# Kernel optimization log

Hardware: AMD Instinct MI355X
Metric: run time of the kernel (lower is better)

## Reference

```python
import jax, jax.numpy as jnp
import numpy as np

OUT_H, OUT_W = 7, 7
SPATIAL_SCALE = 0.25
SAMPLING_RATIO = 2  # fixed sampling grid per bin (sampling_ratio > 0 branch)


def setup_inputs() -> dict:
    key = jax.random.key(0)
    k1, k2, k3, k4, k5 = jax.random.split(key, 5)
    B, C, H, W = 2, 256, 200, 200
    N = 1000
    features = jax.random.normal(k1, (B, C, H, W), dtype=jnp.float32)
    # rois: [batch_idx, cx, cy, w, h, theta] in IMAGE coords (image = 800x800 since scale=0.25)
    batch_idx = jax.random.randint(k2, (N,), 0, B).astype(jnp.float32)
    centers = jax.random.uniform(k3, (N, 2), minval=100.0, maxval=700.0)
    sizes = jax.random.uniform(k4, (N, 2), minval=32.0, maxval=256.0)
    angles = jax.random.uniform(k5, (N, 1), minval=0.0, maxval=float(np.pi))
    rois = jnp.concatenate([batch_idx[:, None], centers, sizes, angles], axis=1).astype(jnp.float32)
    return {"features": features, "rois": rois}


def _roi_align_rotated(features, rois, out_h, out_w, scale, g):
    B, C, H, W = features.shape
    N = rois.shape[0]
    b = rois[:, 0].astype(jnp.int32)
    cx = rois[:, 1] * scale
    cy = rois[:, 2] * scale
    rw = jnp.maximum(rois[:, 3] * scale, 1.0)
    rh = jnp.maximum(rois[:, 4] * scale, 1.0)
    theta = rois[:, 5]
    bin_h = rh / out_h
    bin_w = rw / out_w
    # sample offsets within the roi: yy = -h/2 + (s + 0.5) * bin/g for s in [0, out*g)
    sy = (jnp.arange(out_h * g, dtype=features.dtype) + 0.5) / g  # [Hs] in bin units
    sx = (jnp.arange(out_w * g, dtype=features.dtype) + 0.5) / g  # [Ws]
    yy = -rh[:, None] * 0.5 + sy[None, :] * bin_h[:, None]  # [N, Hs]
    xx = -rw[:, None] * 0.5 + sx[None, :] * bin_w[:, None]  # [N, Ws]
    cos_t = jnp.cos(theta)[:, None, None]
    sin_t = jnp.sin(theta)[:, None, None]
    # rotate around roi center (mmcv / detectron2 convention)
    y = yy[:, :, None] * cos_t - xx[:, None, :] * sin_t + cy[:, None, None]  # [N, Hs, Ws]
    x = yy[:, :, None] * sin_t + xx[:, None, :] * cos_t + cx[:, None, None]
    # bilinear_interpolate semantics from the CUDA kernel
    inside = (y >= -1.0) & (y <= H) & (x >= -1.0) & (x <= W)
    yc = jnp.clip(y, 0.0)
    xc = jnp.clip(x, 0.0)
    yl = jnp.minimum(jnp.floor(yc).astype(jnp.int32), H - 1)
    xl = jnp.minimum(jnp.floor(xc).astype(jnp.int32), W - 1)
    yh = jnp.minimum(yl + 1, H - 1)
    xh = jnp.minimum(xl + 1, W - 1)
    ly = jnp.where(jnp.floor(yc) >= H - 1, 0.0, yc - yl)
    lx = jnp.where(jnp.floor(xc) >= W - 1, 0.0, xc - xl)
    hy = 1.0 - ly
    hx = 1.0 - lx
    bi = b[:, None, None]
    v1 = features[bi, :, yl, xl]  # [N, Hs, Ws, C]
    v2 = features[bi, :, yl, xh]
    v3 = features[bi, :, yh, xl]
    v4 = features[bi, :, yh, xh]
    w1 = (hy * hx)[..., None]
    w2 = (hy * lx)[..., None]
    w3 = (ly * hx)[..., None]
    w4 = (ly * lx)[..., None]
    val = w1 * v1 + w2 * v2 + w3 * v3 + w4 * v4
    val = jnp.where(inside[..., None], val, 0.0)
    # average over the g x g samples per output bin
    val = val.reshape(N, out_h, g, out_w, g, C).mean(axis=(2, 4))  # [N, out_h, out_w, C]
    return jnp.transpose(val, (0, 3, 1, 2))  # [N, C, out_h, out_w]


def reference(features, rois):
    return _roi_align_rotated(features, rois, OUT_H, OUT_W, SPATIAL_SCALE, SAMPLING_RATIO)
```

## Files before the change

kernel.cpp:

```cpp
#include <hip/hip_runtime.h>
#include <hip/hip_fp16.h>


#define B_ 2
#define C_ 256
#define H_ 200
#define W_ 200
#define OUTHW 7
#define GRID_S 14
#define NSAMP 196
#define ELEMS (C_ * OUTHW * OUTHW)

__global__ __launch_bounds__(256) void transpose_h_kernel(
    const float* __restrict__ feat, __half* __restrict__ featT)
{
    __shared__ float tile[64][65];
    const int x0   = blockIdx.x * 64;
    const int c0   = blockIdx.y * 64;
    const int yb   = blockIdx.z;
    const int y    = yb % H_;
    const int b    = yb / H_;
    const int t    = threadIdx.x;
    const int lane = t & 63;
    const int grp  = t >> 6;
    const int nx   = min(64, W_ - x0);

    if (lane < nx) {
        #pragma unroll
        for (int i = 0; i < 16; ++i) {
            const int cl = grp * 16 + i;
            tile[cl][lane] =
                feat[((size_t)(b * C_ + c0 + cl) * H_ + y) * W_ + x0 + lane];
        }
    }
    __syncthreads();

    for (int i = grp; i < nx; i += 4) {
        const float v = tile[lane][i];
        featT[((size_t)(b * H_ + y) * W_ + x0 + i) * C_ + c0 + lane] =
            __float2half(v);
    }
}

__device__ __forceinline__ void build_table(
    const float* __restrict__ rois, int n, int t,
    float s_w[4][NSAMP], int s_idx[4][NSAMP], int pix_stride, int fold_batch,
    int* s_b)
{
    const float spatial_scale = 0.25f;
    if (t == 0 && s_b) *s_b = (int)rois[n * 6 + 0];
    if (t < NSAMP) {
        const int   b  = (int)rois[n * 6 + 0];
        const float cx = rois[n * 6 + 1] * spatial_scale;
        const float cy = rois[n * 6 + 2] * spatial_scale;
        const float rw = fmaxf(rois[n * 6 + 3] * spatial_scale, 1.0f);
        const float rh = fmaxf(rois[n * 6 + 4] * spatial_scale, 1.0f);
        const float th = rois[n * 6 + 5];
        const float cosv = cosf(th), sinv = sinf(th);

        const float bin_h = rh * (1.0f / OUTHW);
        const float bin_w = rw * (1.0f / OUTHW);
        const int row = t / GRID_S;
        const int col = t % GRID_S;

        const float yy = -rh * 0.5f + ((float)row + 0.5f) * 0.5f * bin_h;
        const float xx = -rw * 0.5f + ((float)col + 0.5f) * 0.5f * bin_w;

        const float y = yy * cosv - xx * sinv + cy;
        const float x = yy * sinv + xx * cosv + cx;

        const bool inside = (y >= -1.0f) && (y <= (float)H_) &&
                            (x >= -1.0f) && (x <= (float)W_);

        const float yc = fmaxf(y, 0.0f);
        const float xc = fmaxf(x, 0.0f);
        const float fy = floorf(yc);
        const float fx = floorf(xc);
        int yl = min((int)fy, H_ - 1);
        int xl = min((int)fx, W_ - 1);
        const int yh = min(yl + 1, H_ - 1);
        const int xh = min(xl + 1, W_ - 1);
        const float ly = (fy >= (float)(H_ - 1)) ? 0.0f : (yc - fy);
        const float lx = (fx >= (float)(W_ - 1)) ? 0.0f : (xc - fx);
        const float hy = 1.0f - ly;
        const float hx = 1.0f - lx;

        const float m = inside ? 0.25f : 0.0f;
        s_w[0][t] = hy * hx * m;
        s_w[1][t] = hy * lx * m;
        s_w[2][t] = ly * hx * m;
        s_w[3][t] = ly * lx * m;
        const int bb = fold_batch ? b : 0;
        s_idx[0][t] = ((bb * H_ + yl) * W_ + xl) * pix_stride;
        s_idx[1][t] = ((bb * H_ + yl) * W_ + xh) * pix_stride;
        s_idx[2][t] = ((bb * H_ + yh) * W_ + xl) * pix_stride;
        s_idx[3][t] = ((bb * H_ + yh) * W_ + xh) * pix_stride;
    }
}

__global__ __launch_bounds__(256) void roi_main_nhwc_h(
    const __half* __restrict__ featT,
    const float* __restrict__ rois,
    float* __restrict__ out)
{
    __shared__ float s_w[4][NSAMP];
    __shared__ int   s_idx[4][NSAMP];
    __shared__ float s_out[49][257];

    const int n = blockIdx.x;
    const int t = threadIdx.x;
    build_table(rois, n, t, s_w, s_idx, C_, 1, nullptr);
    __syncthreads();

    const int lane  = t & 63;
    const int wave  = t >> 6;
    const int cbase = lane * 4;

    for (int bin = wave; bin < OUTHW * OUTHW; bin += 4) {
        const int oy = bin / OUTHW;
        const int ox = bin - oy * OUTHW;
        float a0 = 0.f, a1 = 0.f, a2 = 0.f, a3 = 0.f;
        #pragma unroll
        for (int j = 0; j < 2; ++j) {
            #pragma unroll
            for (int i = 0; i < 2; ++i) {
                const int s = (oy * 2 + j) * GRID_S + (ox * 2 + i);
                #pragma unroll
                for (int q = 0; q < 4; ++q) {
                    const float w = s_w[q][s];
                    const __half2* p =
                        (const __half2*)(featT + s_idx[q][s] + cbase);
                    const float2 fa = __half22float2(p[0]);
                    const float2 fb = __half22float2(p[1]);
                    a0 += w * fa.x; a1 += w * fa.y;
                    a2 += w * fb.x; a3 += w * fb.y;
                }
            }
        }
        s_out[bin][0 * 64 + lane] = a0;
        s_out[bin][1 * 64 + lane] = a1;
        s_out[bin][2 * 64 + lane] = a2;
        s_out[bin][3 * 64 + lane] = a3;
    }
    __syncthreads();

    float* __restrict__ ob = out + (size_t)n * ELEMS;
    for (int k = 0; k < 49; ++k) {
        const int e   = t + k * 256;
        const int c   = e / 49;
        const int bin = e - c * 49;
        ob[e] = s_out[bin][(c & 3) * 64 + (c >> 2)];
    }
}

__global__ __launch_bounds__(256) void roi_main_nchw(
    const float* __restrict__ feat,
    const float* __restrict__ rois,
    float* __restrict__ out)
{
    const int n = blockIdx.x;
    const int t = threadIdx.x;
    __shared__ float s_w[4][NSAMP];
    __shared__ int   s_idx[4][NSAMP];
    __shared__ int   s_b;

    build_table(rois, n, t, s_w, s_idx, 1, 0, &s_b);
    __syncthreads();

    const float* __restrict__ fb = feat + (size_t)s_b * (size_t)(C_ * H_ * W_);
    float* __restrict__ ob = out + (size_t)n * (size_t)ELEMS;

    for (int e = t; e < ELEMS; e += 256) {
        const int c   = e / 49;
        const int bin = e - c * 49;
        const int oy  = bin / 7;
        const int ox  = bin - oy * 7;
        const float* __restrict__ fc = fb + c * (H_ * W_);
        float acc = 0.0f;
        #pragma unroll
        for (int j = 0; j < 2; ++j) {
            #pragma unroll
            for (int i = 0; i < 2; ++i) {
                const int s = (oy * 2 + j) * GRID_S + (ox * 2 + i);
                acc += s_w[0][s] * fc[s_idx[0][s]];
                acc += s_w[1][s] * fc[s_idx[1][s]];
                acc += s_w[2][s] * fc[s_idx[2][s]];
                acc += s_w[3][s] * fc[s_idx[3][s]];
            }
        }
        ob[e] = acc;
    }
}

extern "C" void kernel_launch(void* const* d_in, const int* in_sizes, int n_in,
                              void* d_out, int out_size, void* d_ws, size_t ws_size,
                              hipStream_t stream) {
    const float* feat = (const float*)d_in[0];
    const float* rois = (const float*)d_in[1];
    float* out = (float*)d_out;
    const int N = in_sizes[1] / 6;

    const size_t need = (size_t)B_ * H_ * W_ * C_ * sizeof(__half);
    if (ws_size >= need) {
        __half* featT = (__half*)d_ws;
        dim3 tg((W_ + 63) / 64, C_ / 64, H_ * B_);
        transpose_h_kernel<<<tg, 256, 0, stream>>>(feat, featT);
        roi_main_nhwc_h<<<N, 256, 0, stream>>>(featT, rois, out);
    } else {
        roi_main_nchw<<<N, 256, 0, stream>>>(feat, rois, out);
    }
}
```

Before: 185.2 us.

## Vectorize transpose and split ROI output staging into two halves

The transpose kernel now reads float4 and writes packed half4 (8-byte) stores instead of scalar accesses. The main ROI kernel processes the 49 bins in two phases (25 and 24 bins), halving the s_out shared buffer so more blocks can be resident per CU, with a strided scatter to output per phase. Feature gathers use a single 8-byte load instead of two half2 loads. The price is an extra barrier and less contiguous output writes per phase.

Result: slower. 192.1 us (+3.7%).

```diff
diff --git a/kernel.cpp b/kernel.cpp
--- a/kernel.cpp
+++ b/kernel.cpp
@@ -15,30 +15,39 @@
     const float* __restrict__ feat, __half* __restrict__ featT)
 {
     __shared__ float tile[64][65];
-    const int x0   = blockIdx.x * 64;
-    const int c0   = blockIdx.y * 64;
-    const int yb   = blockIdx.z;
-    const int y    = yb % H_;
-    const int b    = yb / H_;
-    const int t    = threadIdx.x;
-    const int lane = t & 63;
-    const int grp  = t >> 6;
-    const int nx   = min(64, W_ - x0);
-
-    if (lane < nx) {
+    const int x0 = blockIdx.x * 64;
+    const int c0 = blockIdx.y * 64;
+    const int yb = blockIdx.z;
+    const int y  = yb % H_;
+    const int b  = yb / H_;
+    const int t  = threadIdx.x;
+    const int nx = min(64, W_ - x0);
+
+    const int rr = t >> 4;
+    const int jj = t & 15;
+    if (jj * 4 < nx) {
         #pragma unroll
-        for (int i = 0; i < 16; ++i) {
-            const int cl = grp * 16 + i;
-            tile[cl][lane] =
-                feat[((size_t)(b * C_ + c0 + cl) * H_ + y) * W_ + x0 + lane];
-        }
-    }
-    __syncthreads();
-
-    for (int i = grp; i < nx; i += 4) {
-        const float v = tile[lane][i];
-        featT[((size_t)(b * H_ + y) * W_ + x0 + i) * C_ + c0 + lane] =
-            __float2half(v);
+        for (int p = 0; p < 4; ++p) {
+            const int cl = p * 16 + rr;
+            const float4 v = *(const float4*)(feat +
+                ((size_t)(b * C_ + c0 + cl) * H_ + y) * W_ + x0 + jj * 4);
+            *(float4*)&tile[cl][jj * 4] = v;
+        }
+    }
+    __syncthreads();
+
+    const int ii = t >> 4;
+    const int cq = (t & 15) * 4;
+    #pragma unroll
+    for (int p = 0; p < 4; ++p) {
+        const int i = p * 16 + ii;
+        if (i < nx) {
+            union { __half2 h2[2]; float2 f2; } u;
+            u.h2[0] = __floats2half2_rn(tile[cq + 0][i], tile[cq + 1][i]);
+            u.h2[1] = __floats2half2_rn(tile[cq + 2][i], tile[cq + 3][i]);
+            *(float2*)(featT +
+                ((size_t)(b * H_ + y) * W_ + x0 + i) * C_ + c0 + cq) = u.f2;
+        }
     }
 }
 
@@ -98,25 +107,15 @@
     }
 }
 
-__global__ __launch_bounds__(256) void roi_main_nhwc_h(
+template <int B0, int BC>
+__device__ __forceinline__ void roi_phase(
     const __half* __restrict__ featT,
-    const float* __restrict__ rois,
-    float* __restrict__ out)
-{
-    __shared__ float s_w[4][NSAMP];
-    __shared__ int   s_idx[4][NSAMP];
-    __shared__ float s_out[49][257];
-
-    const int n = blockIdx.x;
-    const int t = threadIdx.x;
-    build_table(rois, n, t, s_w, s_idx, C_, 1, nullptr);
-    __syncthreads();
-
-    const int lane  = t & 63;
-    const int wave  = t >> 6;
+    const float s_w[4][NSAMP], const int s_idx[4][NSAMP],
+    float s_out[25][257], float* __restrict__ ob,
+    int lane, int wave, int t)
+{
     const int cbase = lane * 4;
-
-    for (int bin = wave; bin < OUTHW * OUTHW; bin += 4) {
+    for (int bin = B0 + wave; bin < B0 + BC; bin += 4) {
         const int oy = bin / OUTHW;
         const int ox = bin - oy * OUTHW;
         float a0 = 0.f, a1 = 0.f, a2 = 0.f, a3 = 0.f;
@@ -128,29 +127,52 @@
                 #pragma unroll
                 for (int q = 0; q < 4; ++q) {
                     const float w = s_w[q][s];
-                    const __half2* p =
-                        (const __half2*)(featT + s_idx[q][s] + cbase);
-                    const float2 fa = __half22float2(p[0]);
-                    const float2 fb = __half22float2(p[1]);
+                    const float2 rv =
+                        *(const float2*)(featT + s_idx[q][s] + cbase);
+                    const __half2* hp = (const __half2*)&rv;
+                    const float2 fa = __half22float2(hp[0]);
+                    const float2 fb = __half22float2(hp[1]);
                     a0 += w * fa.x; a1 += w * fa.y;
                     a2 += w * fb.x; a3 += w * fb.y;
                 }
             }
         }
-        s_out[bin][0 * 64 + lane] = a0;
-        s_out[bin][1 * 64 + lane] = a1;
-        s_out[bin][2 * 64 + lane] = a2;
-        s_out[bin][3 * 64 + lane] = a3;
-    }
-    __syncthreads();
-
+        const int jb = bin - B0;
+        s_out[jb][0 * 64 + lane] = a0;
+        s_out[jb][1 * 64 + lane] = a1;
+        s_out[jb][2 * 64 + lane] = a2;
+        s_out[jb][3 * 64 + lane] = a3;
+    }
+    __syncthreads();
+    #pragma unroll 4
+    for (int m = t; m < BC * 256; m += 256) {
+        const int c = m / BC;
+        const int j = m - c * BC;
+        ob[c * 49 + B0 + j] = s_out[j][(c & 3) * 64 + (c >> 2)];
+    }
+}
+
+__global__ __launch_bounds__(256) void roi_main_nhwc_h(
+    const __half* __restrict__ featT,
+    const float* __restrict__ rois,
+    float* __restrict__ out)
+{
+    __shared__ float s_w[4][NSAMP];
+    __shared__ int   s_idx[4][NSAMP];
+    __shared__ float s_out[25][257];
+
+    const int n = blockIdx.x;
+    const int t = threadIdx.x;
+    build_table(rois, n, t, s_w, s_idx, C_, 1, nullptr);
+    __syncthreads();
+
+    const int lane = t & 63;
+    const int wave = t >> 6;
     float* __restrict__ ob = out + (size_t)n * ELEMS;
-    for (int k = 0; k < 49; ++k) {
-        const int e   = t + k * 256;
-        const int c   = e / 49;
-        const int bin = e - c * 49;
-        ob[e] = s_out[bin][(c & 3) * 64 + (c >> 2)];
-    }
+
+    roi_phase<0, 25>(featT, s_w, s_idx, s_out, ob, lane, wave, t);
+    __syncthreads();
+    roi_phase<25, 24>(featT, s_w, s_idx, s_out, ob, lane, wave, t);
 }
 
 __global__ __launch_bounds__(256) void roi_main_nchw(
```
